# Optimization experiments

Hardware: AMD Instinct MI355X
Metric: run time of the kernel (lower is better)

The kernel has to match this reference:

```python
import jax, jax.numpy as jnp
import numpy as np

N = 50000   # number of points (x = y)
K = 32      # fixed neighborhood size
E = N * K   # total edges in CRS
D = 3       # coordinate dim (d1 = d2)
C = 32      # f_y channels (d3); kernel output must match for 'nonlinear'
H = 64      # MLP hidden width


def setup_inputs() -> dict:
    key = jax.random.key(0)
    ks = jax.random.split(key, 9)
    y = jax.random.normal(ks[0], (N, D), dtype=jnp.float32)
    f_y = jax.random.normal(ks[1], (N, C), dtype=jnp.float32)
    weights = jax.random.uniform(ks[2], (N, 1), dtype=jnp.float32)
    neighbors_index = jax.random.randint(ks[3], (E,), 0, N, dtype=jnp.int32)
    neighbors_row_splits = jnp.arange(N + 1, dtype=jnp.int32) * K
    s1 = 1.0 / np.sqrt(2 * D + C)
    s2 = 1.0 / np.sqrt(H)
    W1 = jax.random.normal(ks[4], (2 * D + C, H), dtype=jnp.float32) * s1
    b1 = jnp.zeros((H,), dtype=jnp.float32)
    W2 = jax.random.normal(ks[5], (H, H), dtype=jnp.float32) * s2
    b2 = jnp.zeros((H,), dtype=jnp.float32)
    W3 = jax.random.normal(ks[6], (H, C), dtype=jnp.float32) * s2
    b3 = jnp.zeros((C,), dtype=jnp.float32)
    return {"y": y, "f_y": f_y, "weights": weights,
            "W1": W1, "b1": b1, "W2": W2, "b2": b2, "W3": W3, "b3": b3,
            "neighbors_index": neighbors_index,
            "neighbors_row_splits": neighbors_row_splits}


def _mlp(h, W1, b1, W2, b2, W3, b3):
    # MLPLinear: Linear -> gelu -> Linear -> gelu -> Linear (no final act).
    # torch F.gelu defaults to exact erf form.
    h = jax.nn.gelu(h @ W1 + b1, approximate=False)
    h = jax.nn.gelu(h @ W2 + b2, approximate=False)
    return h @ W3 + b3


def reference(y, f_y, weights, W1, b1, W2, b2, W3, b3,
              neighbors_index, neighbors_row_splits):
    # x = y (x not given). transform_type='nonlinear' with weights -> sum-reduce.
    e = jnp.arange(neighbors_index.shape[0])
    # segment id for each edge: splits[i] <= e < splits[i+1]
    seg_ids = jnp.searchsorted(neighbors_row_splits, e, side='right') - 1

    rep_features = y[neighbors_index]          # [E, D]  neighbor coords
    in_features = f_y[neighbors_index]         # [E, C]  neighbor features
    self_features = y[seg_ids]                 # [E, D]  repeat_interleave(x)

    agg = jnp.concatenate([rep_features, self_features, in_features], axis=-1)
    k = _mlp(agg, W1, b1, W2, b2, W3, b3)      # [E, C]
    k = k * in_features                        # diagonal kernel * f(y)
    k = weights[neighbors_index] * k           # [E,1] * [E,C]

    num_segments = neighbors_row_splits.shape[0] - 1
    out = jax.ops.segment_sum(k, seg_ids, num_segments=num_segments)  # [N, C]
    return out
```

## Files before the change

### kernel.cpp

```cpp
#include <hip/hip_runtime.h>
#include <hip/hip_bf16.h>
#include <math.h>


typedef __attribute__((ext_vector_type(8))) short short8;
typedef __attribute__((ext_vector_type(4))) float floatx4;

__device__ __forceinline__ unsigned short bf16rne(float f) {
    unsigned int u = __float_as_uint(f);
    u += 0x7fffu + ((u >> 16) & 1u);
    return (unsigned short)(u >> 16);
}
__device__ __forceinline__ unsigned int pk2(float a, float b) {
    union { __hip_bfloat162 h; unsigned int u; } cv;
    cv.h = __float22bfloat162_rn(make_float2(a, b));
    return cv.u;
}
__device__ __forceinline__ float bf16f(unsigned short u) {
    return __uint_as_float(((unsigned int)u) << 16);
}
__device__ __forceinline__ float gelu_fast(float x) {
    float u = x * fmaf(0.044715f * x, x, 1.0f);
    float e = __expf(1.5957691f * u);
    float r = __builtin_amdgcn_rcpf(e + 1.0f);
    return fmaf(-x, r, x);
}

#define MFMA16(a, b, c) __builtin_amdgcn_mfma_f32_16x16x32_bf16(a, b, c, 0, 0, 0)

__global__ __launch_bounds__(256) void cvt_bf16(const float* __restrict__ in,
                                                unsigned short* __restrict__ o16,
                                                int n8) {
    int i = blockIdx.x * 256 + threadIdx.x;
    if (i >= n8) return;
    const float4* p = (const float4*)(in + (size_t)i * 8);
    float4 a = p[0], b = p[1];
    *(uint4*)(o16 + (size_t)i * 8) =
        make_uint4(pk2(a.x, a.y), pk2(a.z, a.w), pk2(b.x, b.y), pk2(b.z, b.w));
}

__global__ __launch_bounds__(256) void pack_weights(
    const float* __restrict__ W1, const float* __restrict__ W2,
    const float* __restrict__ W3, unsigned short* __restrict__ wpack)
{
    int t = blockIdx.x * 256 + threadIdx.x;
    if (t >= 20 * 64) return;
    int f = t >> 6, lane = t & 63;
    int quad = lane >> 4, c16 = lane & 15;
    unsigned short v8[8];
    if (f < 8) {
        int kb = f >> 2, nb = f & 3;
        #pragma unroll
        for (int j = 0; j < 8; ++j) {
            int kp = kb * 32 + quad * 8 + j;
            int n  = nb * 16 + c16;
            int r  = (kp < 32) ? (6 + kp) : (kp < 38 ? kp - 32 : -1);
            v8[j] = (r >= 0) ? bf16rne(W1[r * 64 + n]) : (unsigned short)0;
        }
    } else if (f < 16) {
        int kb = (f - 8) >> 2, nb = (f - 8) & 3;
        #pragma unroll
        for (int j = 0; j < 8; ++j) {
            int k = kb * 32 + quad * 8 + j;
            v8[j] = bf16rne(W2[k * 64 + nb * 16 + c16]);
        }
    } else {
        int kb = (f - 16) >> 1, nb = (f - 16) & 1;
        #pragma unroll
        for (int j = 0; j < 8; ++j) {
            int k = kb * 32 + quad * 8 + j;
            v8[j] = bf16rne(W3[k * 32 + nb * 16 + c16]);
        }
    }
    uint4 o;
    o.x = (unsigned)v8[0] | ((unsigned)v8[1] << 16);
    o.y = (unsigned)v8[2] | ((unsigned)v8[3] << 16);
    o.z = (unsigned)v8[4] | ((unsigned)v8[5] << 16);
    o.w = (unsigned)v8[6] | ((unsigned)v8[7] << 16);
    *(uint4*)(wpack + (size_t)t * 8) = o;
}

__global__ __launch_bounds__(256, 4) void it_mfma(
    const float* __restrict__ y, const unsigned short* __restrict__ fy16,
    const float* __restrict__ wts,
    const unsigned short* __restrict__ wpack,
    const float* __restrict__ b1, const float* __restrict__ b2,
    const float* __restrict__ b3,
    const int* __restrict__ nbr,
    float* __restrict__ out, int npts)
{
    __shared__ unsigned short wlds[20 * 64 * 8];
    __shared__ unsigned short ldsB[4][32][72];

    const int tid  = threadIdx.x;
    const int lane = tid & 63;
    const int wv   = tid >> 6;
    const int quad = lane >> 4;
    const int c16  = lane & 15;
    const int wgid   = blockIdx.x * 4 + wv;
    const int nwaves = gridDim.x * 4;

    {
        const uint4* src = (const uint4*)wpack;
        uint4* dst = (uint4*)wlds;
        #pragma unroll
        for (int i = 0; i < 5; ++i)
            dst[tid + i * 256] = src[tid + i * 256];
    }
    __syncthreads();
    if (wgid >= npts) return;

    float b1v[4], b2v[4], b3v[2];
    #pragma unroll
    for (int nb = 0; nb < 4; ++nb) { b1v[nb] = b1[nb * 16 + c16]; b2v[nb] = b2[nb * 16 + c16]; }
    b3v[0] = b3[c16]; b3v[1] = b3[16 + c16];

    unsigned short (*bufB)[72] = ldsB[wv];
    const floatx4 fz = {0.f, 0.f, 0.f, 0.f};

    int p = wgid;
    int   e32 = nbr[p * 32 + (lane & 31)];
    float w32 = wts[e32];
    short8 a0c[2];
    float yjc[2][3] = {{0.f,0.f,0.f},{0.f,0.f,0.f}};
    {
        int j0 = __shfl(e32, c16), j1 = __shfl(e32, 16 + c16);
        a0c[0] = *(const short8*)(fy16 + (size_t)j0 * 32 + quad * 8);
        a0c[1] = *(const short8*)(fy16 + (size_t)j1 * 32 + quad * 8);
        if (quad == 0) {
            yjc[0][0] = y[3*j0]; yjc[0][1] = y[3*j0+1]; yjc[0][2] = y[3*j0+2];
            yjc[1][0] = y[3*j1]; yjc[1][1] = y[3*j1+1]; yjc[1][2] = y[3*j1+2];
        }
    }
    float yjn[2][3] = {{0.f,0.f,0.f},{0.f,0.f,0.f}};

    unsigned woff = 0;

    for (;;) {
        asm volatile("" : "+v"(woff));
        const unsigned short* wp = wlds + woff;
        #define WFRAG(fid) (*(const short8*)(wp + (((fid) * 64 + lane) * 8)))

        const int pu = __builtin_amdgcn_readfirstlane(p);
        const int pn = p + nwaves;
        const bool last = (pn >= npts);
        const int pnc = last ? p : pn;
        int e32n = nbr[pnc * 32 + (lane & 31)];

        const float yi0 = y[3*pu], yi1 = y[3*pu+1], yi2 = y[3*pu+2];

        #pragma unroll
        for (int t = 0; t < 2; ++t) {
            short8 a1 = {0,0,0,0,0,0,0,0};
            if (quad == 0) {
                union { short8 s; unsigned int u[4]; } cv;
                cv.u[0] = pk2(yjc[t][0], yjc[t][1]);
                cv.u[1] = pk2(yjc[t][2], yi0);
                cv.u[2] = pk2(yi1, yi2);
                cv.u[3] = 0u;
                a1 = cv.s;
            }
            floatx4 acc[4];
            #pragma unroll
            for (int nb = 0; nb < 4; ++nb) {
                acc[nb] = MFMA16(a0c[t], WFRAG(nb), fz);
                acc[nb] = MFMA16(a1,     WFRAG(4 + nb), acc[nb]);
            }
            #pragma unroll
            for (int r = 0; r < 4; ++r) {
                float g0 = gelu_fast(acc[0][r] + b1v[0]);
                float g1 = gelu_fast(acc[1][r] + b1v[1]);
                float g2 = gelu_fast(acc[2][r] + b1v[2]);
                float g3 = gelu_fast(acc[3][r] + b1v[3]);
                unsigned int p01 = pk2(g0, g1), p23 = pk2(g2, g3);
                int orow = t * 16 + quad * 4 + r;
                bufB[orow][c16]      = (unsigned short)p01;
                bufB[orow][16 + c16] = (unsigned short)(p01 >> 16);
                bufB[orow][32 + c16] = (unsigned short)p23;
                bufB[orow][48 + c16] = (unsigned short)(p23 >> 16);
            }
        }

        unsigned short f0r[2][4], f1r[2][4];
        float wrr[2][4];
        #pragma unroll
        for (int r = 0; r < 4; ++r) {
            int orow = quad * 4 + r;
            int jr = __shfl(e32, orow);
            f0r[0][r] = fy16[(size_t)jr * 32 + c16];
            f1r[0][r] = fy16[(size_t)jr * 32 + 16 + c16];
            wrr[0][r] = __shfl(w32, orow);
        }

        short8 a0n[2];
        float w32n;
        {
            int jn0 = __shfl(e32n, c16), jn1 = __shfl(e32n, 16 + c16);
            a0n[0] = *(const short8*)(fy16 + (size_t)jn0 * 32 + quad * 8);
            a0n[1] = *(const short8*)(fy16 + (size_t)jn1 * 32 + quad * 8);
            w32n = wts[e32n];
            if (quad == 0) {
                yjn[0][0] = y[3*jn0]; yjn[0][1] = y[3*jn0+1]; yjn[0][2] = y[3*jn0+2];
                yjn[1][0] = y[3*jn1]; yjn[1][1] = y[3*jn1+1]; yjn[1][2] = y[3*jn1+2];
            }
        }

        float colsum0 = 0.f, colsum1 = 0.f;
        #pragma unroll
        for (int t = 0; t < 2; ++t) {
            if (t == 1) {
                #pragma unroll
                for (int r = 0; r < 4; ++r) {
                    int orow = 16 + quad * 4 + r;
                    int jr = __shfl(e32, orow);
                    f0r[1][r] = fy16[(size_t)jr * 32 + c16];
                    f1r[1][r] = fy16[(size_t)jr * 32 + 16 + c16];
                    wrr[1][r] = __shfl(w32, orow);
                }
            }
            const int arow = t * 16 + c16;
            short8 h0 = *(const short8*)&bufB[arow][quad * 8];
            short8 h1 = *(const short8*)&bufB[arow][32 + quad * 8];
            floatx4 acc[4];
            #pragma unroll
            for (int nb = 0; nb < 4; ++nb) {
                acc[nb] = MFMA16(h0, WFRAG(8 + nb), fz);
                acc[nb] = MFMA16(h1, WFRAG(12 + nb), acc[nb]);
            }
            #pragma unroll
            for (int r = 0; r < 4; ++r) {
                float g0 = gelu_fast(acc[0][r] + b2v[0]);
                float g1 = gelu_fast(acc[1][r] + b2v[1]);
                float g2 = gelu_fast(acc[2][r] + b2v[2]);
                float g3 = gelu_fast(acc[3][r] + b2v[3]);
                unsigned int p01 = pk2(g0, g1), p23 = pk2(g2, g3);
                int orow = t * 16 + quad * 4 + r;
                bufB[orow][c16]      = (unsigned short)p01;
                bufB[orow][16 + c16] = (unsigned short)(p01 >> 16);
                bufB[orow][32 + c16] = (unsigned short)p23;
                bufB[orow][48 + c16] = (unsigned short)(p23 >> 16);
            }
            short8 g0s = *(const short8*)&bufB[arow][quad * 8];
            short8 g1s = *(const short8*)&bufB[arow][32 + quad * 8];
            floatx4 o[2];
            #pragma unroll
            for (int nb = 0; nb < 2; ++nb) {
                o[nb] = MFMA16(g0s, WFRAG(16 + nb), fz);
                o[nb] = MFMA16(g1s, WFRAG(18 + nb), o[nb]);
            }
            #pragma unroll
            for (int r = 0; r < 4; ++r) {
                colsum0 = fmaf((o[0][r] + b3v[0]) * bf16f(f0r[t][r]), wrr[t][r], colsum0);
                colsum1 = fmaf((o[1][r] + b3v[1]) * bf16f(f1r[t][r]), wrr[t][r], colsum1);
            }
        }
        #undef WFRAG

        colsum0 += __shfl_xor(colsum0, 16, 64);
        colsum0 += __shfl_xor(colsum0, 32, 64);
        colsum1 += __shfl_xor(colsum1, 16, 64);
        colsum1 += __shfl_xor(colsum1, 32, 64);
        if (lane < 32)
            out[pu * 32 + lane] = (lane < 16) ? colsum0 : colsum1;

        if (last) break;
        p = pn;
        e32 = e32n; w32 = w32n;
        a0c[0] = a0n[0]; a0c[1] = a0n[1];
        #pragma unroll
        for (int t = 0; t < 2; ++t)
            #pragma unroll
            for (int k = 0; k < 3; ++k) yjc[t][k] = yjn[t][k];
    }
}

extern "C" void kernel_launch(void* const* d_in, const int* in_sizes, int n_in,
                              void* d_out, int out_size, void* d_ws, size_t ws_size,
                              hipStream_t stream) {
    const float* y  = (const float*)d_in[0];
    const float* fy = (const float*)d_in[1];
    const float* wt = (const float*)d_in[2];
    const float* W1 = (const float*)d_in[3];
    const float* b1 = (const float*)d_in[4];
    const float* W2 = (const float*)d_in[5];
    const float* b2 = (const float*)d_in[6];
    const float* W3 = (const float*)d_in[7];
    const float* b3 = (const float*)d_in[8];
    const int* nbr  = (const int*)d_in[9];
    const int E = in_sizes[9];
    const int npts = E >> 5;
    float* out = (float*)d_out;

    unsigned short* wpack = (unsigned short*)d_ws;
    unsigned short* fy16  = (unsigned short*)((char*)d_ws + 32768);

    hipLaunchKernelGGL(pack_weights, dim3(5), dim3(256), 0, stream,
                       W1, W2, W3, wpack);
    const int n8 = npts * 4;
    hipLaunchKernelGGL(cvt_bf16, dim3((n8 + 255) / 256), dim3(256), 0, stream,
                       fy, fy16, n8);

    static int bpc = 0;
    if (bpc == 0) {
        hipOccupancyMaxActiveBlocksPerMultiprocessor(&bpc, it_mfma, 256, 0);
        if (bpc < 1) bpc = 3;
        if (bpc > 8) bpc = 8;
    }
    int grid = bpc * 256;
    hipLaunchKernelGGL(it_mfma, dim3(grid), dim3(256), 0, stream,
                       y, fy16, wt, wpack, b1, b2, b3, nbr, out, npts);
}
```

Baseline: 199.8 us.

## Compute MLP transposed and pass activations via lane butterflies instead of LDS

Swaps the MFMA operand order so weights become the A operand and edge activations the B operand. Each layer's GELU output can then be rearranged with cross-lane butterfly shuffles into the next layer's input fragment, with no round trip through per-wave LDS scratch. The first-layer bias is folded into the W1 matrix through a constant-1 input column. The b2 and b3 biases move into a permuted table in LDS, and GELU is evaluated in paired float2 form. The output reduction becomes a 16-lane shuffle tree with float4 stores, and LDS scratch use drops, at the cost of more shuffles and bias reads from LDS on every iteration.

```diff
diff --git a/kernel.cpp b/kernel.cpp
--- a/kernel.cpp
+++ b/kernel.cpp
@@ -5,6 +5,8 @@
 
 typedef __attribute__((ext_vector_type(8))) short short8;
 typedef __attribute__((ext_vector_type(4))) float floatx4;
+typedef __attribute__((ext_vector_type(2))) float f32x2;
+typedef __attribute__((ext_vector_type(4))) unsigned short ushort4v;
 
 __device__ __forceinline__ unsigned short bf16rne(float f) {
     unsigned int u = __float_as_uint(f);
@@ -19,14 +21,25 @@
 __device__ __forceinline__ float bf16f(unsigned short u) {
     return __uint_as_float(((unsigned int)u) << 16);
 }
-__device__ __forceinline__ float gelu_fast(float x) {
-    float u = x * fmaf(0.044715f * x, x, 1.0f);
-    float e = __expf(1.5957691f * u);
-    float r = __builtin_amdgcn_rcpf(e + 1.0f);
-    return fmaf(-x, r, x);
+__device__ __forceinline__ f32x2 gelu2(f32x2 x) {
+    f32x2 t = x * x;
+    f32x2 u = x * (0.044715f * t + 1.0f);
+    float ex = __expf(1.5957691f * u.x);
+    float ey = __expf(1.5957691f * u.y);
+    f32x2 r;
+    r.x = __builtin_amdgcn_rcpf(ex + 1.0f);
+    r.y = __builtin_amdgcn_rcpf(ey + 1.0f);
+    return x - x * r;
 }
 
 #define MFMA16(a, b, c) __builtin_amdgcn_mfma_f32_16x16x32_bf16(a, b, c, 0, 0, 0)
+
+#define BFLY(L, X0, X1) {                                   \
+    int t0_ = __shfl_xor((int)(X0), (L), 64);               \
+    int t1_ = __shfl_xor((int)(X1), (L), 64);               \
+    unsigned n0_ = (lane & (L)) ? (unsigned)t1_ : (X0);     \
+    unsigned n1_ = (lane & (L)) ? (X1) : (unsigned)t0_;     \
+    (X0) = n0_; (X1) = n1_; }
 
 __global__ __launch_bounds__(256) void cvt_bf16(const float* __restrict__ in,
                                                 unsigned short* __restrict__ o16,
@@ -40,57 +53,69 @@
 }
 
 __global__ __launch_bounds__(256) void pack_weights(
-    const float* __restrict__ W1, const float* __restrict__ W2,
-    const float* __restrict__ W3, unsigned short* __restrict__ wpack)
+    const float* __restrict__ W1, const float* __restrict__ b1,
+    const float* __restrict__ W2, const float* __restrict__ b2,
+    const float* __restrict__ W3, const float* __restrict__ b3,
+    unsigned short* __restrict__ wpack)
 {
     int t = blockIdx.x * 256 + threadIdx.x;
-    if (t >= 20 * 64) return;
-    int f = t >> 6, lane = t & 63;
-    int quad = lane >> 4, c16 = lane & 15;
-    unsigned short v8[8];
-    if (f < 8) {
-        int kb = f >> 2, nb = f & 3;
-        #pragma unroll
-        for (int j = 0; j < 8; ++j) {
-            int kp = kb * 32 + quad * 8 + j;
-            int n  = nb * 16 + c16;
-            int r  = (kp < 32) ? (6 + kp) : (kp < 38 ? kp - 32 : -1);
-            v8[j] = (r >= 0) ? bf16rne(W1[r * 64 + n]) : (unsigned short)0;
-        }
-    } else if (f < 16) {
-        int kb = (f - 8) >> 2, nb = (f - 8) & 3;
-        #pragma unroll
-        for (int j = 0; j < 8; ++j) {
-            int k = kb * 32 + quad * 8 + j;
-            v8[j] = bf16rne(W2[k * 64 + nb * 16 + c16]);
-        }
-    } else {
-        int kb = (f - 16) >> 1, nb = (f - 16) & 1;
-        #pragma unroll
-        for (int j = 0; j < 8; ++j) {
-            int k = kb * 32 + quad * 8 + j;
-            v8[j] = bf16rne(W3[k * 32 + nb * 16 + c16]);
-        }
-    }
-    uint4 o;
-    o.x = (unsigned)v8[0] | ((unsigned)v8[1] << 16);
-    o.y = (unsigned)v8[2] | ((unsigned)v8[3] << 16);
-    o.z = (unsigned)v8[4] | ((unsigned)v8[5] << 16);
-    o.w = (unsigned)v8[6] | ((unsigned)v8[7] << 16);
-    *(uint4*)(wpack + (size_t)t * 8) = o;
+    if (t < 20 * 64) {
+        int f = t >> 6, lane = t & 63;
+        int quad = lane >> 4, c16 = lane & 15;
+        unsigned short v8[8];
+        if (f < 8) {
+            int kb = f >> 2, nb = f & 3;
+            #pragma unroll
+            for (int j = 0; j < 8; ++j) {
+                int kp = kb * 32 + quad * 8 + j;
+                int n  = nb * 16 + c16;
+                float v;
+                if (kp < 32)      v = W1[(6 + kp) * 64 + n];
+                else if (kp < 38) v = W1[(kp - 32) * 64 + n];
+                else if (kp == 38) v = b1[n];
+                else              v = 0.f;
+                v8[j] = bf16rne(v);
+            }
+        } else if (f < 16) {
+            int kb = (f - 8) >> 2, nb = (f - 8) & 3;
+            #pragma unroll
+            for (int j = 0; j < 8; ++j) {
+                int k = kb * 32 + quad * 8 + j;
+                v8[j] = bf16rne(W2[k * 64 + nb * 16 + c16]);
+            }
+        } else {
+            int kb = (f - 16) >> 1, nb = (f - 16) & 1;
+            #pragma unroll
+            for (int j = 0; j < 8; ++j) {
+                int k = kb * 32 + quad * 8 + j;
+                v8[j] = bf16rne(W3[k * 32 + nb * 16 + c16]);
+            }
+        }
+        uint4 o;
+        o.x = (unsigned)v8[0] | ((unsigned)v8[1] << 16);
+        o.y = (unsigned)v8[2] | ((unsigned)v8[3] << 16);
+        o.z = (unsigned)v8[4] | ((unsigned)v8[5] << 16);
+        o.w = (unsigned)v8[6] | ((unsigned)v8[7] << 16);
+        *(uint4*)(wpack + (size_t)t * 8) = o;
+    } else if (t < 1344) {
+        int idx = t - 1280;
+        float* btab = (float*)(wpack + 10240);
+        btab[idx] = b2[16 * ((idx >> 2) & 3) + 4 * (idx >> 4) + (idx & 3)];
+    } else if (t < 1376) {
+        int idx = t - 1344;
+        float* btab = (float*)(wpack + 10240);
+        btab[64 + idx] = b3[16 * ((idx >> 2) & 1) + 4 * (idx >> 3) + (idx & 3)];
+    }
 }
 
 __global__ __launch_bounds__(256, 4) void it_mfma(
     const float* __restrict__ y, const unsigned short* __restrict__ fy16,
     const float* __restrict__ wts,
     const unsigned short* __restrict__ wpack,
-    const float* __restrict__ b1, const float* __restrict__ b2,
-    const float* __restrict__ b3,
     const int* __restrict__ nbr,
     float* __restrict__ out, int npts)
 {
-    __shared__ unsigned short wlds[20 * 64 * 8];
-    __shared__ unsigned short ldsB[4][32][72];
+    __shared__ unsigned short wlds[10432];
 
     const int tid  = threadIdx.x;
     const int lane = tid & 63;
@@ -104,18 +129,14 @@
         const uint4* src = (const uint4*)wpack;
         uint4* dst = (uint4*)wlds;
         #pragma unroll
-        for (int i = 0; i < 5; ++i)
-            dst[tid + i * 256] = src[tid + i * 256];
+        for (int i = 0; i < 6; ++i) {
+            int idx = tid + i * 256;
+            if (idx < 1304) dst[idx] = src[idx];
+        }
     }
     __syncthreads();
     if (wgid >= npts) return;
 
-    float b1v[4], b2v[4], b3v[2];
-    #pragma unroll
-    for (int nb = 0; nb < 4; ++nb) { b1v[nb] = b1[nb * 16 + c16]; b2v[nb] = b2[nb * 16 + c16]; }
-    b3v[0] = b3[c16]; b3v[1] = b3[16 + c16];
-
-    unsigned short (*bufB)[72] = ldsB[wv];
     const floatx4 fz = {0.f, 0.f, 0.f, 0.f};
 
     int p = wgid;
@@ -133,12 +154,15 @@
         }
     }
     float yjn[2][3] = {{0.f,0.f,0.f},{0.f,0.f,0.f}};
+    short8 a0n[2];
+    float w32n = 0.f;
 
     unsigned woff = 0;
 
     for (;;) {
         asm volatile("" : "+v"(woff));
         const unsigned short* wp = wlds + woff;
+        const float* bp = (const float*)((const char*)wp + 20480);
         #define WFRAG(fid) (*(const short8*)(wp + (((fid) * 64 + lane) * 8)))
 
         const int pu = __builtin_amdgcn_readfirstlane(p);
@@ -148,6 +172,16 @@
         int e32n = nbr[pnc * 32 + (lane & 31)];
 
         const float yi0 = y[3*pu], yi1 = y[3*pu+1], yi2 = y[3*pu+2];
+
+        floatx4 b2v[4], b3v[2];
+        #pragma unroll
+        for (int mb = 0; mb < 4; ++mb)
+            b2v[mb] = *(const floatx4*)(bp + quad * 16 + mb * 4);
+        b3v[0] = *(const floatx4*)(bp + 64 + quad * 8);
+        b3v[1] = *(const floatx4*)(bp + 64 + quad * 8 + 4);
+
+        float vs0[4] = {0.f, 0.f, 0.f, 0.f};
+        float vs1[4] = {0.f, 0.f, 0.f, 0.f};
 
         #pragma unroll
         for (int t = 0; t < 2; ++t) {
@@ -157,111 +191,107 @@
                 cv.u[0] = pk2(yjc[t][0], yjc[t][1]);
                 cv.u[1] = pk2(yjc[t][2], yi0);
                 cv.u[2] = pk2(yi1, yi2);
-                cv.u[3] = 0u;
+                cv.u[3] = pk2(1.0f, 0.0f);
                 a1 = cv.s;
             }
             floatx4 acc[4];
             #pragma unroll
-            for (int nb = 0; nb < 4; ++nb) {
-                acc[nb] = MFMA16(a0c[t], WFRAG(nb), fz);
-                acc[nb] = MFMA16(a1,     WFRAG(4 + nb), acc[nb]);
-            }
+            for (int mb = 0; mb < 4; ++mb) {
+                acc[mb] = MFMA16(WFRAG(mb),     a0c[t], fz);
+                acc[mb] = MFMA16(WFRAG(4 + mb), a1,     acc[mb]);
+            }
+            unsigned uu[8];
+            #pragma unroll
+            for (int mb = 0; mb < 4; ++mb)
+                #pragma unroll
+                for (int r1 = 0; r1 < 2; ++r1) {
+                    f32x2 xin = {acc[mb][2*r1], acc[mb][2*r1+1]};
+                    f32x2 g = gelu2(xin);
+                    uu[mb*2 + r1] = pk2(g.x, g.y);
+                }
+            BFLY(32, uu[0], uu[2]); BFLY(32, uu[1], uu[3]);
+            BFLY(32, uu[4], uu[6]); BFLY(32, uu[5], uu[7]);
+            BFLY(16, uu[0], uu[2]); BFLY(16, uu[1], uu[3]);
+            BFLY(16, uu[4], uu[6]); BFLY(16, uu[5], uu[7]);
+            short8 hb0, hb1;
+            {
+                union { unsigned u[4]; short8 s; } c0, c1;
+                c0.u[0]=uu[0]; c0.u[1]=uu[1]; c0.u[2]=uu[2]; c0.u[3]=uu[3];
+                c1.u[0]=uu[4]; c1.u[1]=uu[5]; c1.u[2]=uu[6]; c1.u[3]=uu[7];
+                hb0 = c0.s; hb1 = c1.s;
+            }
+            #pragma unroll
+            for (int mb = 0; mb < 4; ++mb) {
+                acc[mb] = MFMA16(WFRAG(8 + mb),  hb0, fz);
+                acc[mb] = MFMA16(WFRAG(12 + mb), hb1, acc[mb]);
+            }
+            #pragma unroll
+            for (int mb = 0; mb < 4; ++mb)
+                #pragma unroll
+                for (int r1 = 0; r1 < 2; ++r1) {
+                    f32x2 xin = {acc[mb][2*r1]   + b2v[mb][2*r1],
+                                 acc[mb][2*r1+1] + b2v[mb][2*r1+1]};
+                    f32x2 g = gelu2(xin);
+                    uu[mb*2 + r1] = pk2(g.x, g.y);
+                }
+            BFLY(32, uu[0], uu[2]); BFLY(32, uu[1], uu[3]);
+            BFLY(32, uu[4], uu[6]); BFLY(32, uu[5], uu[7]);
+            BFLY(16, uu[0], uu[2]); BFLY(16, uu[1], uu[3]);
+            BFLY(16, uu[4], uu[6]); BFLY(16, uu[5], uu[7]);
+            short8 gb0, gb1;
+            {
+                union { unsigned u[4]; short8 s; } c0, c1;
+                c0.u[0]=uu[0]; c0.u[1]=uu[1]; c0.u[2]=uu[2]; c0.u[3]=uu[3];
+                c1.u[0]=uu[4]; c1.u[1]=uu[5]; c1.u[2]=uu[6]; c1.u[3]=uu[7];
+                gb0 = c0.s; gb1 = c1.s;
+            }
+            floatx4 o0, o1;
+            o0 = MFMA16(WFRAG(16), gb0, fz);
+            o0 = MFMA16(WFRAG(18), gb1, o0);
+            o1 = MFMA16(WFRAG(17), gb0, fz);
+            o1 = MFMA16(WFRAG(19), gb1, o1);
+
+            if (t == 0) {
+                int jn0 = __shfl(e32n, c16), jn1 = __shfl(e32n, 16 + c16);
+                a0n[0] = *(const short8*)(fy16 + (size_t)jn0 * 32 + quad * 8);
+                a0n[1] = *(const short8*)(fy16 + (size_t)jn1 * 32 + quad * 8);
+                w32n = wts[e32n];
+                if (quad == 0) {
+                    yjn[0][0] = y[3*jn0]; yjn[0][1] = y[3*jn0+1]; yjn[0][2] = y[3*jn0+2];
+                    yjn[1][0] = y[3*jn1]; yjn[1][1] = y[3*jn1+1]; yjn[1][2] = y[3*jn1+2];
+                }
+            }
+
+            int   el = t * 16 + c16;
+            int   je = __shfl(e32, el);
+            float we = __shfl(w32, el);
+            ushort4v fa = *(const ushort4v*)(fy16 + (size_t)je * 32 + 4 * quad);
+            ushort4v fb = *(const ushort4v*)(fy16 + (size_t)je * 32 + 16 + 4 * quad);
             #pragma unroll
             for (int r = 0; r < 4; ++r) {
-                float g0 = gelu_fast(acc[0][r] + b1v[0]);
-                float g1 = gelu_fast(acc[1][r] + b1v[1]);
-                float g2 = gelu_fast(acc[2][r] + b1v[2]);
-                float g3 = gelu_fast(acc[3][r] + b1v[3]);
-                unsigned int p01 = pk2(g0, g1), p23 = pk2(g2, g3);
-                int orow = t * 16 + quad * 4 + r;
-                bufB[orow][c16]      = (unsigned short)p01;
-                bufB[orow][16 + c16] = (unsigned short)(p01 >> 16);
-                bufB[orow][32 + c16] = (unsigned short)p23;
-                bufB[orow][48 + c16] = (unsigned short)(p23 >> 16);
-            }
-        }
-
-        unsigned short f0r[2][4], f1r[2][4];
-        float wrr[2][4];
+                vs0[r] = fmaf((o0[r] + b3v[0][r]) * bf16f(fa[r]), we, vs0[r]);
+                vs1[r] = fmaf((o1[r] + b3v[1][r]) * bf16f(fb[r]), we, vs1[r]);
+            }
+        }
+        #undef WFRAG
+
         #pragma unroll
         for (int r = 0; r < 4; ++r) {
-            int orow = quad * 4 + r;
-            int jr = __shfl(e32, orow);
-            f0r[0][r] = fy16[(size_t)jr * 32 + c16];
-            f1r[0][r] = fy16[(size_t)jr * 32 + 16 + c16];
-            wrr[0][r] = __shfl(w32, orow);
-        }
-
-        short8 a0n[2];
-        float w32n;
-        {
-            int jn0 = __shfl(e32n, c16), jn1 = __shfl(e32n, 16 + c16);
-            a0n[0] = *(const short8*)(fy16 + (size_t)jn0 * 32 + quad * 8);
-            a0n[1] = *(const short8*)(fy16 + (size_t)jn1 * 32 + quad * 8);
-            w32n = wts[e32n];
-            if (quad == 0) {
-                yjn[0][0] = y[3*jn0]; yjn[0][1] = y[3*jn0+1]; yjn[0][2] = y[3*jn0+2];
-                yjn[1][0] = y[3*jn1]; yjn[1][1] = y[3*jn1+1]; yjn[1][2] = y[3*jn1+2];
-            }
-        }
-
-        float colsum0 = 0.f, colsum1 = 0.f;
-        #pragma unroll
-        for (int t = 0; t < 2; ++t) {
-            if (t == 1) {
-                #pragma unroll
-                for (int r = 0; r < 4; ++r) {
-                    int orow = 16 + quad * 4 + r;
-                    int jr = __shfl(e32, orow);
-                    f0r[1][r] = fy16[(size_t)jr * 32 + c16];
-                    f1r[1][r] = fy16[(size_t)jr * 32 + 16 + c16];
-                    wrr[1][r] = __shfl(w32, orow);
-                }
-            }
-            const int arow = t * 16 + c16;
-            short8 h0 = *(const short8*)&bufB[arow][quad * 8];
-            short8 h1 = *(const short8*)&bufB[arow][32 + quad * 8];
-            floatx4 acc[4];
-            #pragma unroll
-            for (int nb = 0; nb < 4; ++nb) {
-                acc[nb] = MFMA16(h0, WFRAG(8 + nb), fz);
-                acc[nb] = MFMA16(h1, WFRAG(12 + nb), acc[nb]);
-            }
-            #pragma unroll
-            for (int r = 0; r < 4; ++r) {
-                float g0 = gelu_fast(acc[0][r] + b2v[0]);
-                float g1 = gelu_fast(acc[1][r] + b2v[1]);
-                float g2 = gelu_fast(acc[2][r] + b2v[2]);
-                float g3 = gelu_fast(acc[3][r] + b2v[3]);
-                unsigned int p01 = pk2(g0, g1), p23 = pk2(g2, g3);
-                int orow = t * 16 + quad * 4 + r;
-                bufB[orow][c16]      = (unsigned short)p01;
-                bufB[orow][16 + c16] = (unsigned short)(p01 >> 16);
-                bufB[orow][32 + c16] = (unsigned short)p23;
-                bufB[orow][48 + c16] = (unsigned short)(p23 >> 16);
-            }
-            short8 g0s = *(const short8*)&bufB[arow][quad * 8];
-            short8 g1s = *(const short8*)&bufB[arow][32 + quad * 8];
-            floatx4 o[2];
-            #pragma unroll
-            for (int nb = 0; nb < 2; ++nb) {
-                o[nb] = MFMA16(g0s, WFRAG(16 + nb), fz);
-                o[nb] = MFMA16(g1s, WFRAG(18 + nb), o[nb]);
-            }
-            #pragma unroll
-            for (int r = 0; r < 4; ++r) {
-                colsum0 = fmaf((o[0][r] + b3v[0]) * bf16f(f0r[t][r]), wrr[t][r], colsum0);
-                colsum1 = fmaf((o[1][r] + b3v[1]) * bf16f(f1r[t][r]), wrr[t][r], colsum1);
-            }
-        }
-        #undef WFRAG
-
-        colsum0 += __shfl_xor(colsum0, 16, 64);
-        colsum0 += __shfl_xor(colsum0, 32, 64);
-        colsum1 += __shfl_xor(colsum1, 16, 64);
-        colsum1 += __shfl_xor(colsum1, 32, 64);
-        if (lane < 32)
-            out[pu * 32 + lane] = (lane < 16) ? colsum0 : colsum1;
+            vs0[r] += __shfl_xor(vs0[r], 1, 64);
+            vs0[r] += __shfl_xor(vs0[r], 2, 64);
+            vs0[r] += __shfl_xor(vs0[r], 4, 64);
+            vs0[r] += __shfl_xor(vs0[r], 8, 64);
+            vs1[r] += __shfl_xor(vs1[r], 1, 64);
+            vs1[r] += __shfl_xor(vs1[r], 2, 64);
+            vs1[r] += __shfl_xor(vs1[r], 4, 64);
+            vs1[r] += __shfl_xor(vs1[r], 8, 64);
+        }
+        if (c16 == 0) {
+            *(float4*)(out + (size_t)pu * 32 + 4 * quad) =
+                make_float4(vs0[0], vs0[1], vs0[2], vs0[3]);
+            *(float4*)(out + (size_t)pu * 32 + 16 + 4 * quad) =
+                make_float4(vs1[0], vs1[1], vs1[2], vs1[3]);
+        }
 
         if (last) break;
         p = pn;
@@ -294,8 +324,8 @@
     unsigned short* wpack = (unsigned short*)d_ws;
     unsigned short* fy16  = (unsigned short*)((char*)d_ws + 32768);
 
-    hipLaunchKernelGGL(pack_weights, dim3(5), dim3(256), 0, stream,
-                       W1, W2, W3, wpack);
+    hipLaunchKernelGGL(pack_weights, dim3(6), dim3(256), 0, stream,
+                       W1, b1, W2, b2, W3, b3, wpack);
     const int n8 = npts * 4;
     hipLaunchKernelGGL(cvt_bf16, dim3((n8 + 255) / 256), dim3(256), 0, stream,
                        fy, fy16, n8);
@@ -303,10 +333,10 @@
     static int bpc = 0;
     if (bpc == 0) {
         hipOccupancyMaxActiveBlocksPerMultiprocessor(&bpc, it_mfma, 256, 0);
-        if (bpc < 1) bpc = 3;
+        if (bpc < 1) bpc = 4;
         if (bpc > 8) bpc = 8;
     }
     int grid = bpc * 256;
     hipLaunchKernelGGL(it_mfma, dim3(grid), dim3(256), 0, stream,
-                       y, fy16, wt, wpack, b1, b2, b3, nbr, out, npts);
-}
+                       y, fy16, wt, wpack, nbr, out, npts);
+}
```

Measured after the change: 223.9 us. 12.1% more time.
